# Kernel optimization log

Hardware: AMD Instinct MI355X
Metric: run time of the kernel (lower is better)

Reference implementation:

```python
import jax, jax.numpy as jnp
import numpy as np

N = 50000
E = 800000
IN_DIM = 256
HID = 32
HEADS = 4
OUT_DIM = 40
NEG_SLOPE = 0.2


def gat_layer(x, src, dst, W, a_src, a_dst, b, n_nodes, heads, ch, concat):
    # x: [N, F_in], W: [F_in, heads*ch], a_src/a_dst: [heads, ch], b: [out]
    h = (x @ W).reshape(n_nodes, heads, ch)                 # [N,H,C]
    alpha_s = jnp.einsum('nhc,hc->nh', h, a_src)            # [N,H]
    alpha_d = jnp.einsum('nhc,hc->nh', h, a_dst)            # [N,H]
    e = jax.nn.leaky_relu(alpha_s[src] + alpha_d[dst], NEG_SLOPE)  # [E,H]
    # segment softmax over destination neighborhoods (self-loops guarantee nonempty)
    m = jax.ops.segment_max(e, dst, num_segments=n_nodes)   # [N,H]
    e = jnp.exp(e - m[dst])
    denom = jax.ops.segment_sum(e, dst, num_segments=n_nodes)
    alpha = e / (denom[dst] + 1e-16)                         # [E,H]
    msg = h[src] * alpha[:, :, None]                         # [E,H,C]
    out = jax.ops.segment_sum(msg, dst, num_segments=n_nodes)  # [N,H,C]
    out = out.reshape(n_nodes, heads * ch) if concat else out.mean(axis=1)
    return out + b


def setup_inputs() -> dict:
    key = jax.random.key(0)
    ks = jax.random.split(key, 10)
    x = jax.random.normal(ks[0], (N, IN_DIM), dtype=jnp.float32)
    edge_index = jax.random.randint(ks[1], (2, E), 0, N, dtype=jnp.int32)
    s1 = 1.0 / np.sqrt(IN_DIM)
    s2 = 1.0 / np.sqrt(HID * HEADS)
    return {
        'x': x,
        'edge_index': edge_index,
        'W1': jax.random.normal(ks[2], (IN_DIM, HEADS * HID), dtype=jnp.float32) * s1,
        'a_src1': jax.random.normal(ks[3], (HEADS, HID), dtype=jnp.float32) * s1,
        'a_dst1': jax.random.normal(ks[4], (HEADS, HID), dtype=jnp.float32) * s1,
        'b1': jnp.zeros((HEADS * HID,), dtype=jnp.float32),
        'W2': jax.random.normal(ks[5], (HEADS * HID, OUT_DIM), dtype=jnp.float32) * s2,
        'a_src2': jax.random.normal(ks[6], (1, OUT_DIM), dtype=jnp.float32) * s2,
        'a_dst2': jax.random.normal(ks[7], (1, OUT_DIM), dtype=jnp.float32) * s2,
        'b2': jnp.zeros((OUT_DIM,), dtype=jnp.float32),
    }


def reference(x, edge_index, W1, a_src1, a_dst1, b1, W2, a_src2, a_dst2, b2):
    # PyG GATConv adds self-loops by default
    loops = jnp.arange(N, dtype=edge_index.dtype)
    src = jnp.concatenate([edge_index[0], loops])
    dst = jnp.concatenate([edge_index[1], loops])
    h = gat_layer(x, src, dst, W1, a_src1, a_dst1, b1, N, HEADS, HID, True)
    h = jax.nn.relu(h)
    out = gat_layer(h, src, dst, W2, a_src2, a_dst2, b2, N, 1, OUT_DIM, False)
    return jax.nn.log_softmax(out, axis=1)
```

## Files before the change

### kernel.cpp

```cpp
#include <hip/hip_runtime.h>
#include <math.h>

#define N_NODES 50000
#define N_EDGES 800000
#define IN_DIM  256
#define F1      128
#define HEADS   4
#define OUT_DIM 40
#define NEG     0.2f

#define NB   391
#define CAP  3072
#define EB   4096

#define DCAP 96

typedef __attribute__((ext_vector_type(8))) short short8;
typedef __attribute__((ext_vector_type(4))) float float4v;

__device__ __forceinline__ unsigned short f2bf(float f) {
  unsigned int u = __float_as_uint(f);
  u += 0x7FFF + ((u >> 16) & 1);
  return (unsigned short)(u >> 16);
}
__device__ __forceinline__ float bf2f(unsigned short h) {
  return __uint_as_float((unsigned int)h << 16);
}
__device__ __forceinline__ float bflo(unsigned int u) { return __uint_as_float(u << 16); }
__device__ __forceinline__ float bfhi(unsigned int u) { return __uint_as_float(u & 0xffff0000u); }

__device__ __forceinline__ float lrelu(float e) { return e > 0.f ? e : e * NEG; }

__global__ __launch_bounds__(256) void bin_kernel(const int* __restrict__ ei,
                                                  int* __restrict__ gcnt,
                                                  int2* __restrict__ gbucket) {
  __shared__ int ls[EB];
  __shared__ int ld[EB];
  __shared__ int lcnt[NB];
  __shared__ int lcur[NB];
  __shared__ int gbaseS[NB];
  int tid = threadIdx.x;
  size_t base = (size_t)blockIdx.x * EB;
  for (int t = tid; t < NB; t += 256) { lcnt[t] = 0; lcur[t] = 0; }
  __syncthreads();
#pragma unroll
  for (int l = 0; l < EB / 256; l++) {
    int li = l * 256 + tid;
    size_t idx = base + li;
    int s = 0, d = -1;
    if (idx < N_EDGES) {
      s = ei[idx];
      d = ei[N_EDGES + idx];
      atomicAdd(&lcnt[d >> 7], 1);
    }
    ls[li] = s;
    ld[li] = d;
  }
  __syncthreads();
  for (int t = tid; t < NB; t += 256) gbaseS[t] = atomicAdd(&gcnt[t], lcnt[t]);
  __syncthreads();
#pragma unroll
  for (int l = 0; l < EB / 256; l++) {
    int li = l * 256 + tid;
    int d = ld[li];
    if (d >= 0) {
      int b = d >> 7;
      int r = gbaseS[b] + atomicAdd(&lcur[b], 1);
      if (r >= CAP) r = CAP - 1;
      gbucket[(size_t)b * CAP + r] = make_int2(ls[li], d);
    }
  }
}

__global__ __launch_bounds__(512) void bucketscan_kernel(const int* __restrict__ gcnt,
                                                         int* __restrict__ bbase,
                                                         int* __restrict__ row_ptr) {
  __shared__ int lds[512];
  int tid = threadIdx.x;
  int v = (tid < NB) ? gcnt[tid] : 0;
  lds[tid] = v;
  __syncthreads();
  for (int off = 1; off < 512; off <<= 1) {
    int t = (tid >= off) ? lds[tid - off] : 0;
    __syncthreads();
    lds[tid] += t;
    __syncthreads();
  }
  if (tid < NB) bbase[tid] = lds[tid] - v;
  if (tid == 0) row_ptr[N_NODES] = N_EDGES;
}

__global__ __launch_bounds__(256) void csr_kernel(const int2* __restrict__ gbucket,
                                                  const int* __restrict__ gcnt,
                                                  const int* __restrict__ bbase,
                                                  int* __restrict__ row_ptr,
                                                  int* __restrict__ col) {
  __shared__ int2 ent[CAP];
  __shared__ int hcnt[128];
  __shared__ int sc[128];
  __shared__ int cur[128];
  int b = blockIdx.x;
  int tid = threadIdx.x;
  int cnt = gcnt[b]; if (cnt > CAP) cnt = CAP;
  int base = bbase[b];
  if (tid < 128) hcnt[tid] = 0;
  __syncthreads();
  for (int i = tid; i < cnt; i += 256) {
    int2 e = gbucket[(size_t)b * CAP + i];
    ent[i] = e;
    atomicAdd(&hcnt[e.y & 127], 1);
  }
  __syncthreads();
  if (tid < 128) sc[tid] = hcnt[tid];
  __syncthreads();
  for (int off = 1; off < 128; off <<= 1) {
    int t = 0;
    if (tid < 128 && tid >= off) t = sc[tid - off];
    __syncthreads();
    if (tid < 128) sc[tid] += t;
    __syncthreads();
  }
  if (tid < 128) {
    int excl = sc[tid] - hcnt[tid];
    cur[tid] = excl;
    int node = (b << 7) + tid;
    if (node < N_NODES) row_ptr[node] = base + excl;
  }
  __syncthreads();
  for (int i = tid; i < cnt; i += 256) {
    int2 e = ent[i];
    int r = atomicAdd(&cur[e.y & 127], 1);
    col[base + r] = e.x;
  }
}

__global__ __launch_bounds__(256) void w1pack_kernel(const float* __restrict__ W1,
                                                     unsigned short* __restrict__ wHi,
                                                     unsigned short* __restrict__ wLo) {
  int tid = blockIdx.x * 256 + threadIdx.x;
  int kk = tid >> 9;
  int rest = tid & 511;
  int t = rest >> 6;
  int lane = rest & 63;
  int q = lane >> 4;
  int ln = lane & 15;
  int n = t * 16 + ln;
  unsigned int hi[4], lo[4];
#pragma unroll
  for (int jj = 0; jj < 4; jj++) {
    unsigned short h0, h1, l0, l1;
    {
      float v = W1[(kk * 32 + q * 8 + jj * 2) * F1 + n];
      h0 = f2bf(v); l0 = f2bf(v - bf2f(h0));
    }
    {
      float v = W1[(kk * 32 + q * 8 + jj * 2 + 1) * F1 + n];
      h1 = f2bf(v); l1 = f2bf(v - bf2f(h1));
    }
    hi[jj] = (unsigned int)h0 | ((unsigned int)h1 << 16);
    lo[jj] = (unsigned int)l0 | ((unsigned int)l1 << 16);
  }
  size_t base = (size_t)tid * 8;
  *(uint4*)&wHi[base] = make_uint4(hi[0], hi[1], hi[2], hi[3]);
  *(uint4*)&wLo[base] = make_uint4(lo[0], lo[1], lo[2], lo[3]);
}

__global__ __launch_bounds__(256, 3) void gemm1_mfma_kernel(
    const float* __restrict__ x, const unsigned short* __restrict__ wHi,
    const unsigned short* __restrict__ wLo,
    const float* __restrict__ a_src, const float* __restrict__ a_dst,
    unsigned short* __restrict__ h1b, float* __restrict__ as1, float* __restrict__ ad1) {
  int tid = threadIdx.x;
  int w = tid >> 6;
  int lane = tid & 63;
  int q = lane >> 4;
  int ln = lane & 15;
  int rowBase = blockIdx.x * 64 + w * 16;
  int rowA = rowBase + ln;
  int rowAc = rowA < N_NODES ? rowA : N_NODES - 1;
  float4v acc[8];
#pragma unroll
  for (int t = 0; t < 8; t++) acc[t] = (float4v){0.f, 0.f, 0.f, 0.f};
  const short8* bhp = (const short8*)wHi;
  const short8* blp = (const short8*)wLo;
  const float4* xbase = (const float4*)(x + (size_t)rowAc * IN_DIM + q * 8);
  float4 a0 = xbase[0];
  float4 a1 = xbase[1];
#pragma unroll 1
  for (int kk = 0; kk < 8; kk++) {
    short8 bh[8], bl[8];
    int fbase = (kk * 8) * 64 + lane;
#pragma unroll
    for (int t = 0; t < 8; t++) {
      bh[t] = bhp[fbase + t * 64];
      bl[t] = blp[fbase + t * 64];
    }
    int kn = (kk < 7) ? kk + 1 : 7;
    float4 n0 = xbase[kn * 8];
    float4 n1 = xbase[kn * 8 + 1];
    float av[8] = {a0.x, a0.y, a0.z, a0.w, a1.x, a1.y, a1.z, a1.w};
    short8 ahi, alo;
#pragma unroll
    for (int j = 0; j < 8; j++) {
      unsigned short hh = f2bf(av[j]);
      ahi[j] = (short)hh;
      alo[j] = (short)f2bf(av[j] - bf2f(hh));
    }
#pragma unroll
    for (int t = 0; t < 8; t++) {
      acc[t] = __builtin_amdgcn_mfma_f32_16x16x32_bf16(ahi, bh[t], acc[t], 0, 0, 0);
      acc[t] = __builtin_amdgcn_mfma_f32_16x16x32_bf16(ahi, bl[t], acc[t], 0, 0, 0);
      acc[t] = __builtin_amdgcn_mfma_f32_16x16x32_bf16(alo, bh[t], acc[t], 0, 0, 0);
    }
    a0 = n0;
    a1 = n1;
  }
  float asv[8], adv[8];
#pragma unroll
  for (int t = 0; t < 8; t++) {
    asv[t] = a_src[t * 16 + ln];
    adv[t] = a_dst[t * 16 + ln];
  }
#pragma unroll
  for (int reg = 0; reg < 4; reg++) {
    int r = rowBase + q * 4 + reg;
    bool valid = (r < N_NODES);
    if (valid) {
#pragma unroll
      for (int t = 0; t < 8; t++)
        h1b[(size_t)r * F1 + t * 16 + ln] = f2bf(acc[t][reg]);
    }
#pragma unroll
    for (int h = 0; h < 4; h++) {
      float sa = acc[2 * h][reg] * asv[2 * h] + acc[2 * h + 1][reg] * asv[2 * h + 1];
      float sd = acc[2 * h][reg] * adv[2 * h] + acc[2 * h + 1][reg] * adv[2 * h + 1];
#pragma unroll
      for (int off = 1; off < 16; off <<= 1) {
        sa += __shfl_xor(sa, off);
        sd += __shfl_xor(sd, off);
      }
      if (ln == 0 && valid) {
        as1[r * 4 + h] = sa;
        ad1[r * 4 + h] = sd;
      }
    }
  }
}

__global__ __launch_bounds__(256) void gather1_kernel(
    const unsigned short* __restrict__ h1b, const float* __restrict__ as1,
    const float* __restrict__ ad1, const float* __restrict__ b1,
    const int* __restrict__ row_ptr, const int* __restrict__ col,
    float* __restrict__ x2) {
  __shared__ float4 wsh[4][DCAP];
  __shared__ int ssh[4][DCAP];
  int wv = threadIdx.x >> 6;
  int n = blockIdx.x * 4 + wv;
  if (n >= N_NODES) return;
  int lane = threadIdx.x & 63;
  int start = row_ptr[n];
  int deg = row_ptr[n + 1] - start;
  bool fast = (deg + 1) <= DCAP;
  float4 ad = *(const float4*)&ad1[n * 4];
  float s0 = 0.f, s1 = 0.f, s2 = 0.f, s3 = 0.f;
  for (int i = lane; i <= deg; i += 64) {
    int src = (i < deg) ? col[start + i] : n;
    float4 as = *(const float4*)&as1[src * 4];
    float e0 = __expf(lrelu(as.x + ad.x));
    float e1 = __expf(lrelu(as.y + ad.y));
    float e2 = __expf(lrelu(as.z + ad.z));
    float e3 = __expf(lrelu(as.w + ad.w));
    s0 += e0; s1 += e1; s2 += e2; s3 += e3;
    if (fast) {
      ssh[wv][i] = src;
      wsh[wv][i] = make_float4(e0, e1, e2, e3);
    }
  }
#pragma unroll
  for (int off = 32; off > 0; off >>= 1) {
    s0 += __shfl_xor(s0, off);
    s1 += __shfl_xor(s1, off);
    s2 += __shfl_xor(s2, off);
    s3 += __shfl_xor(s3, off);
  }
  int slot = lane >> 4;
  int lane16 = lane & 15;
  int head = lane16 >> 2;
  float rsh = (head == 0) ? s0 : (head == 1) ? s1 : (head == 2) ? s2 : s3;
  rsh = 1.f / (rsh + 1e-16f);
  float4 accA = make_float4(0.f, 0.f, 0.f, 0.f);
  float4 accB = make_float4(0.f, 0.f, 0.f, 0.f);
  if (fast) {
    const float* wp = (const float*)&wsh[wv][0];
    int i = slot;
    for (; i + 4 <= deg; i += 8) {
      int sA = ssh[wv][i];
      int sB = ssh[wv][i + 4];
      float wA = wp[i * 4 + head] * rsh;
      float wB = wp[(i + 4) * 4 + head] * rsh;
      uint4 uA = *(const uint4*)(h1b + (size_t)sA * F1 + lane16 * 8);
      uint4 uB = *(const uint4*)(h1b + (size_t)sB * F1 + lane16 * 8);
      accA.x += wA * bflo(uA.x); accA.y += wA * bfhi(uA.x);
      accA.z += wA * bflo(uA.y); accA.w += wA * bfhi(uA.y);
      accB.x += wA * bflo(uA.z); accB.y += wA * bfhi(uA.z);
      accB.z += wA * bflo(uA.w); accB.w += wA * bfhi(uA.w);
      accA.x += wB * bflo(uB.x); accA.y += wB * bfhi(uB.x);
      accA.z += wB * bflo(uB.y); accA.w += wB * bfhi(uB.y);
      accB.x += wB * bflo(uB.z); accB.y += wB * bfhi(uB.z);
      accB.z += wB * bflo(uB.w); accB.w += wB * bfhi(uB.w);
    }
    if (i <= deg) {
      int s = ssh[wv][i];
      float w = wp[i * 4 + head] * rsh;
      uint4 u = *(const uint4*)(h1b + (size_t)s * F1 + lane16 * 8);
      accA.x += w * bflo(u.x); accA.y += w * bfhi(u.x);
      accA.z += w * bflo(u.y); accA.w += w * bfhi(u.y);
      accB.x += w * bflo(u.z); accB.y += w * bfhi(u.z);
      accB.z += w * bflo(u.w); accB.w += w * bfhi(u.w);
    }
  } else {
    float adh = (head == 0) ? ad.x : (head == 1) ? ad.y : (head == 2) ? ad.z : ad.w;
    for (int i = slot; i <= deg; i += 4) {
      int src = (i < deg) ? col[start + i] : n;
      float w = __expf(lrelu(as1[src * 4 + head] + adh)) * rsh;
      uint4 u = *(const uint4*)(h1b + (size_t)src * F1 + lane16 * 8);
      accA.x += w * bflo(u.x); accA.y += w * bfhi(u.x);
      accA.z += w * bflo(u.y); accA.w += w * bfhi(u.y);
      accB.x += w * bflo(u.z); accB.y += w * bfhi(u.z);
      accB.z += w * bflo(u.w); accB.w += w * bfhi(u.w);
    }
  }
#pragma unroll
  for (int off = 16; off <= 32; off <<= 1) {
    accA.x += __shfl_xor(accA.x, off); accA.y += __shfl_xor(accA.y, off);
    accA.z += __shfl_xor(accA.z, off); accA.w += __shfl_xor(accA.w, off);
    accB.x += __shfl_xor(accB.x, off); accB.y += __shfl_xor(accB.y, off);
    accB.z += __shfl_xor(accB.z, off); accB.w += __shfl_xor(accB.w, off);
  }
  if (slot == 0) {
    float4 bA = *(const float4*)&b1[lane16 * 8];
    float4 bB = *(const float4*)&b1[lane16 * 8 + 4];
    float4 oA, oB;
    oA.x = fmaxf(accA.x + bA.x, 0.f); oA.y = fmaxf(accA.y + bA.y, 0.f);
    oA.z = fmaxf(accA.z + bA.z, 0.f); oA.w = fmaxf(accA.w + bA.w, 0.f);
    oB.x = fmaxf(accB.x + bB.x, 0.f); oB.y = fmaxf(accB.y + bB.y, 0.f);
    oB.z = fmaxf(accB.z + bB.z, 0.f); oB.w = fmaxf(accB.w + bB.w, 0.f);
    *(float4*)&x2[(size_t)n * F1 + lane16 * 8] = oA;
    *(float4*)&x2[(size_t)n * F1 + lane16 * 8 + 4] = oB;
  }
}

__global__ __launch_bounds__(256) void gemm2_kernel(
    const float* __restrict__ x2, const float* __restrict__ W2,
    const float* __restrict__ asv, const float* __restrict__ adv,
    unsigned short* __restrict__ h2b, float* __restrict__ as2, float* __restrict__ ad2) {
  __shared__ float xs[64][132];
  __shared__ float W2s[128][44];
  __shared__ float asv_s[40], adv_s[40];
  int tid = threadIdx.x;
  int bm = blockIdx.x * 64;
#pragma unroll
  for (int l = 0; l < 8; l++) {
    int idx = tid + l * 256;
    int r = idx >> 5;
    int c4 = (idx & 31) << 2;
    float4 v = make_float4(0.f, 0.f, 0.f, 0.f);
    if (bm + r < N_NODES) v = *(const float4*)&x2[(size_t)(bm + r) * F1 + c4];
    *(float4*)&xs[r][c4] = v;
  }
#pragma unroll
  for (int l = 0; l < 5; l++) {
    int idx = tid + l * 256;
    int k = idx / 10;
    int c4 = (idx - k * 10) * 4;
    *(float4*)&W2s[k][c4] = *(const float4*)&W2[k * OUT_DIM + c4];
  }
  if (tid < OUT_DIM) { asv_s[tid] = asv[tid]; adv_s[tid] = adv[tid]; }
  __syncthreads();
  int r = tid >> 2;
  int cb = (tid & 3) * 10;
  float acc[10] = {0.f};
  for (int k = 0; k < F1; k++) {
    float xv = xs[r][k];
#pragma unroll
    for (int c = 0; c < 10; c++) acc[c] += xv * W2s[k][cb + c];
  }
  int grow = bm + r;
  float sa = 0.f, sd = 0.f;
#pragma unroll
  for (int c = 0; c < 10; c++) {
    sa += acc[c] * asv_s[cb + c];
    sd += acc[c] * adv_s[cb + c];
  }
#pragma unroll
  for (int off = 1; off < 4; off <<= 1) {
    sa += __shfl_xor(sa, off);
    sd += __shfl_xor(sd, off);
  }
  if (grow < N_NODES) {
#pragma unroll
    for (int c = 0; c < 10; c += 2) {
      unsigned int p = ((unsigned int)f2bf(acc[c + 1]) << 16) | f2bf(acc[c]);
      *(unsigned int*)&h2b[(size_t)grow * OUT_DIM + cb + c] = p;
    }
    if ((tid & 3) == 0) { as2[grow] = sa; ad2[grow] = sd; }
  }
}

__global__ __launch_bounds__(256) void gather2_kernel(
    const unsigned short* __restrict__ h2b, const float* __restrict__ as2,
    const float* __restrict__ ad2, const float* __restrict__ b2,
    const int* __restrict__ row_ptr, const int* __restrict__ col,
    float* __restrict__ out) {
  __shared__ float w2sh[4][DCAP];
  __shared__ int s2sh[4][DCAP];
  int wv = threadIdx.x >> 6;
  int n = blockIdx.x * 4 + wv;
  if (n >= N_NODES) return;
  int lane = threadIdx.x & 63;
  int start = row_ptr[n];
  int deg = row_ptr[n + 1] - start;
  bool fast = (deg + 1) <= DCAP;
  float adh = ad2[n];
  float part = 0.f;
  for (int i = lane; i <= deg; i += 64) {
    int src = (i < deg) ? col[start + i] : n;
    float e = __expf(lrelu(as2[src] + adh));
    part += e;
    if (fast) { s2sh[wv][i] = src; w2sh[wv][i] = e; }
  }
#pragma unroll
  for (int off = 32; off > 0; off >>= 1) part += __shfl_xor(part, off);
  float rs = 1.f / (part + 1e-16f);
  int slot = lane / 5;
  int c = lane - slot * 5;
  float4 accA = make_float4(0.f, 0.f, 0.f, 0.f);
  float4 accB = make_float4(0.f, 0.f, 0.f, 0.f);
  if (slot < 12) {
    if (fast) {
      for (int i = slot; i <= deg; i += 12) {
        int src = s2sh[wv][i];
        float wgt = w2sh[wv][i] * rs;
        uint4 u = *(const uint4*)(h2b + (size_t)src * OUT_DIM + c * 8);
        accA.x += wgt * bflo(u.x); accA.y += wgt * bfhi(u.x);
        accA.z += wgt * bflo(u.y); accA.w += wgt * bfhi(u.y);
        accB.x += wgt * bflo(u.z); accB.y += wgt * bfhi(u.z);
        accB.z += wgt * bflo(u.w); accB.w += wgt * bfhi(u.w);
      }
    } else {
      for (int i = slot; i <= deg; i += 12) {
        int src = (i < deg) ? col[start + i] : n;
        float wgt = __expf(lrelu(as2[src] + adh)) * rs;
        uint4 u = *(const uint4*)(h2b + (size_t)src * OUT_DIM + c * 8);
        accA.x += wgt * bflo(u.x); accA.y += wgt * bfhi(u.x);
        accA.z += wgt * bflo(u.y); accA.w += wgt * bfhi(u.y);
        accB.x += wgt * bflo(u.z); accB.y += wgt * bfhi(u.z);
        accB.z += wgt * bflo(u.w); accB.w += wgt * bfhi(u.w);
      }
    }
  }
  {
    float v[8] = {accA.x, accA.y, accA.z, accA.w, accB.x, accB.y, accB.z, accB.w};
#pragma unroll
    for (int k = 0; k < 8; k++) v[k] += __shfl(v[k], lane + 30);
#pragma unroll
    for (int k = 0; k < 8; k++) v[k] += __shfl(v[k], lane + 15);
    float t1[8], t2[8];
#pragma unroll
    for (int k = 0; k < 8; k++) t1[k] = __shfl(v[k], lane + 5);
#pragma unroll
    for (int k = 0; k < 8; k++) t2[k] = __shfl(v[k], lane + 10);
#pragma unroll
    for (int k = 0; k < 8; k++) v[k] += t1[k] + t2[k];
    accA.x = v[0]; accA.y = v[1]; accA.z = v[2]; accA.w = v[3];
    accB.x = v[4]; accB.y = v[5]; accB.z = v[6]; accB.w = v[7];
  }
  bool owner = (slot == 0);
  float vals[8] = {accA.x, accA.y, accA.z, accA.w, accB.x, accB.y, accB.z, accB.w};
  float lmax = -1e30f, lsum = 0.f;
  if (owner) {
#pragma unroll
    for (int k = 0; k < 8; k++) {
      vals[k] += b2[c * 8 + k];
      lmax = fmaxf(lmax, vals[k]);
    }
  }
  float gmax = lmax;
#pragma unroll
  for (int off = 32; off > 0; off >>= 1) gmax = fmaxf(gmax, __shfl_xor(gmax, off));
  if (owner) {
#pragma unroll
    for (int k = 0; k < 8; k++) lsum += __expf(vals[k] - gmax);
  }
#pragma unroll
  for (int off = 32; off > 0; off >>= 1) lsum += __shfl_xor(lsum, off);
  if (owner) {
    float lse = gmax + __logf(lsum);
    float4 oA = make_float4(vals[0] - lse, vals[1] - lse, vals[2] - lse, vals[3] - lse);
    float4 oB = make_float4(vals[4] - lse, vals[5] - lse, vals[6] - lse, vals[7] - lse);
    *(float4*)&out[(size_t)n * OUT_DIM + c * 8] = oA;
    *(float4*)&out[(size_t)n * OUT_DIM + c * 8 + 4] = oB;
  }
}

extern "C" void kernel_launch(void* const* d_in, const int* in_sizes, int n_in,
                              void* d_out, int out_size, void* d_ws, size_t ws_size,
                              hipStream_t stream) {
  const float* x      = (const float*)d_in[0];
  const int*   ei     = (const int*)d_in[1];
  const float* W1     = (const float*)d_in[2];
  const float* a_src1 = (const float*)d_in[3];
  const float* a_dst1 = (const float*)d_in[4];
  const float* b1     = (const float*)d_in[5];
  const float* W2     = (const float*)d_in[6];
  const float* a_src2 = (const float*)d_in[7];
  const float* a_dst2 = (const float*)d_in[8];
  const float* b2     = (const float*)d_in[9];
  float* out = (float*)d_out;

  char* ws = (char*)d_ws;
  size_t off = 0;
  auto alloc = [&](size_t bytes) -> void* {
    void* p = ws + off;
    off += (bytes + 255) & ~(size_t)255;
    return p;
  };
  unsigned short* h1b = (unsigned short*)alloc((size_t)N_NODES * F1 * 2);
  unsigned short* h2b = (unsigned short*)alloc((size_t)N_NODES * OUT_DIM * 2);
  unsigned short* wHi = (unsigned short*)alloc((size_t)IN_DIM * F1 * 2);
  unsigned short* wLo = (unsigned short*)alloc((size_t)IN_DIM * F1 * 2);
  float* as1    = (float*)alloc((size_t)N_NODES * HEADS * 4);
  float* ad1    = (float*)alloc((size_t)N_NODES * HEADS * 4);
  float* x2     = (float*)alloc((size_t)N_NODES * F1 * 4);
  float* as2    = (float*)alloc((size_t)N_NODES * 4);
  float* ad2    = (float*)alloc((size_t)N_NODES * 4);
  int* row_ptr  = (int*)alloc((size_t)(N_NODES + 1) * 4);
  int* col      = (int*)alloc((size_t)N_EDGES * 4);
  int* gcnt     = (int*)alloc((size_t)NB * 4);
  int* bbase    = (int*)alloc((size_t)NB * 4);
  int2* gbucket = (int2*)alloc((size_t)NB * CAP * 8);

  hipMemsetAsync(gcnt, 0, (size_t)NB * 4, stream);
  bin_kernel<<<(N_EDGES + EB - 1) / EB, 256, 0, stream>>>(ei, gcnt, gbucket);
  bucketscan_kernel<<<1, 512, 0, stream>>>(gcnt, bbase, row_ptr);
  csr_kernel<<<NB, 256, 0, stream>>>(gbucket, gcnt, bbase, row_ptr, col);

  w1pack_kernel<<<16, 256, 0, stream>>>(W1, wHi, wLo);
  gemm1_mfma_kernel<<<(N_NODES + 63) / 64, 256, 0, stream>>>(
      x, wHi, wLo, a_src1, a_dst1, h1b, as1, ad1);
  gather1_kernel<<<(N_NODES + 3) / 4, 256, 0, stream>>>(h1b, as1, ad1, b1, row_ptr, col, x2);

  gemm2_kernel<<<(N_NODES + 63) / 64, 256, 0, stream>>>(x2, W2, a_src2, a_dst2, h2b, as2, ad2);
  gather2_kernel<<<(N_NODES + 3) / 4, 256, 0, stream>>>(h2b, as2, ad2, b2, row_ptr, col, out);
}
```

Before: 260.5 us.

## Stage GEMM1 weight tiles through double-buffered LDS via direct global-to-LDS loads

Instead of every wave loading the full hi/lo bf16 weight tiles from global memory into registers, the block now cooperatively loads each k-slice into a double-buffered LDS array using global_load_lds, prefetching the next slice while computing the current one. Each wave reads B fragments from LDS, cutting redundant global/L2 traffic fourfold and register pressure. It adds per-iteration barriers and 32KB LDS, and drops the occupancy hint from launch bounds. The correctness of the pipeline relies on the single barrier per iteration covering both the async LDS writes and the reads of the old buffer.

```diff
diff --git a/kernel.cpp b/kernel.cpp
--- a/kernel.cpp
+++ b/kernel.cpp
@@ -30,6 +30,12 @@
 __device__ __forceinline__ float bfhi(unsigned int u) { return __uint_as_float(u & 0xffff0000u); }
 
 __device__ __forceinline__ float lrelu(float e) { return e > 0.f ? e : e * NEG; }
+
+__device__ __forceinline__ void gload_lds16(const void* g, void* l) {
+  __builtin_amdgcn_global_load_lds(
+      (const __attribute__((address_space(1))) unsigned int*)g,
+      (__attribute__((address_space(3))) unsigned int*)l, 16, 0, 0);
+}
 
 __global__ __launch_bounds__(256) void bin_kernel(const int* __restrict__ ei,
                                                   int* __restrict__ gcnt,
@@ -165,11 +171,12 @@
   *(uint4*)&wLo[base] = make_uint4(lo[0], lo[1], lo[2], lo[3]);
 }
 
-__global__ __launch_bounds__(256, 3) void gemm1_mfma_kernel(
+__global__ __launch_bounds__(256) void gemm1_mfma_kernel(
     const float* __restrict__ x, const unsigned short* __restrict__ wHi,
     const unsigned short* __restrict__ wLo,
     const float* __restrict__ a_src, const float* __restrict__ a_dst,
     unsigned short* __restrict__ h1b, float* __restrict__ as1, float* __restrict__ ad1) {
+  __shared__ short8 Bsh[2][1024];
   int tid = threadIdx.x;
   int w = tid >> 6;
   int lane = tid & 63;
@@ -183,18 +190,26 @@
   for (int t = 0; t < 8; t++) acc[t] = (float4v){0.f, 0.f, 0.f, 0.f};
   const short8* bhp = (const short8*)wHi;
   const short8* blp = (const short8*)wLo;
+
+  auto prefetch = [&](int kk, int buf) {
+#pragma unroll
+    for (int c = 0; c < 2; c++) {
+      int chunk = w * 2 + c;
+      gload_lds16(bhp + (size_t)kk * 512 + chunk * 64 + lane, &Bsh[buf][chunk * 64]);
+      gload_lds16(blp + (size_t)kk * 512 + chunk * 64 + lane, &Bsh[buf][512 + chunk * 64]);
+    }
+  };
+
   const float4* xbase = (const float4*)(x + (size_t)rowAc * IN_DIM + q * 8);
   float4 a0 = xbase[0];
   float4 a1 = xbase[1];
+  prefetch(0, 0);
+  __syncthreads();
+
 #pragma unroll 1
   for (int kk = 0; kk < 8; kk++) {
-    short8 bh[8], bl[8];
-    int fbase = (kk * 8) * 64 + lane;
-#pragma unroll
-    for (int t = 0; t < 8; t++) {
-      bh[t] = bhp[fbase + t * 64];
-      bl[t] = blp[fbase + t * 64];
-    }
+    int buf = kk & 1;
+    if (kk < 7) prefetch(kk + 1, buf ^ 1);
     int kn = (kk < 7) ? kk + 1 : 7;
     float4 n0 = xbase[kn * 8];
     float4 n1 = xbase[kn * 8 + 1];
@@ -206,15 +221,20 @@
       ahi[j] = (short)hh;
       alo[j] = (short)f2bf(av[j] - bf2f(hh));
     }
+    const short8* bs = &Bsh[buf][0];
 #pragma unroll
     for (int t = 0; t < 8; t++) {
-      acc[t] = __builtin_amdgcn_mfma_f32_16x16x32_bf16(ahi, bh[t], acc[t], 0, 0, 0);
-      acc[t] = __builtin_amdgcn_mfma_f32_16x16x32_bf16(ahi, bl[t], acc[t], 0, 0, 0);
-      acc[t] = __builtin_amdgcn_mfma_f32_16x16x32_bf16(alo, bh[t], acc[t], 0, 0, 0);
+      short8 bh = bs[t * 64 + lane];
+      short8 bl = bs[512 + t * 64 + lane];
+      acc[t] = __builtin_amdgcn_mfma_f32_16x16x32_bf16(ahi, bh, acc[t], 0, 0, 0);
+      acc[t] = __builtin_amdgcn_mfma_f32_16x16x32_bf16(ahi, bl, acc[t], 0, 0, 0);
+      acc[t] = __builtin_amdgcn_mfma_f32_16x16x32_bf16(alo, bh, acc[t], 0, 0, 0);
     }
     a0 = n0;
     a1 = n1;
-  }
+    if (kk < 7) __syncthreads();
+  }
+
   float asv[8], adv[8];
 #pragma unroll
   for (int t = 0; t < 8; t++) {
```

Measured after the change: 251.0 us. 3.7% less time.
